# Kernel tuning notes

Measured on AMD Instinct MI355X. Metric: run time of the kernel, lower is better.

## Reference

```python
import jax, jax.numpy as jnp
import numpy as np

SEQ_LEN = 512
EMBED_DIM = 768
MAX_SPAN_LEN = 16
WIDTH_EMB_DIM = 50
NUM_SPAN_LABELS = 9
N_SPANS = 32768


def setup_inputs() -> dict:
    key = jax.random.key(0)
    ks = jax.random.split(key, 6)
    sequence_output = jax.random.normal(ks[0], (1, SEQ_LEN, EMBED_DIM), dtype=jnp.float32)
    # start in [0, SEQ_LEN - MAX_SPAN_LEN) so end = start + width stays a valid index
    start_indices = jax.random.randint(ks[1], (N_SPANS,), 0, SEQ_LEN - MAX_SPAN_LEN)
    span_widths = jax.random.randint(ks[2], (N_SPANS,), 1, MAX_SPAN_LEN + 1)  # width >= 1 (mean over non-empty slice)
    end_indices = start_indices + span_widths
    width_table = jax.random.normal(ks[3], (MAX_SPAN_LEN + 1, WIDTH_EMB_DIM), dtype=jnp.float32) * 0.02
    W = jax.random.normal(ks[4], (NUM_SPAN_LABELS, 3 * EMBED_DIM + WIDTH_EMB_DIM), dtype=jnp.float32) * 0.02
    b = jnp.zeros((NUM_SPAN_LABELS,), dtype=jnp.float32)
    return {
        "sequence_output": sequence_output,
        "start_indices": start_indices,
        "end_indices": end_indices,
        "span_widths": span_widths,
        "width_table": width_table,
        "W": W,
        "b": b,
    }


def reference(sequence_output, start_indices, end_indices, span_widths, width_table, W, b):
    # sequence_output: [1, S, D]; batch is asserted to be 1 in the original module.
    seq = sequence_output[0]                       # [S, D]
    h_start = seq[start_indices]                   # [N, D] gather of start tokens
    h_end = seq[end_indices]                       # [N, D] gather of end tokens
    # Ragged mean over seq[s:e] (exclusive end), vectorized via exclusive prefix sums:
    # mean = (cumsum[e] - cumsum[s]) / (e - s)
    cs = jnp.concatenate([jnp.zeros((1, seq.shape[-1]), seq.dtype), jnp.cumsum(seq, axis=0)], axis=0)  # [S+1, D]
    widths_f = span_widths[:, None].astype(seq.dtype)
    h_span_avg = (cs[end_indices] - cs[start_indices]) / widths_f   # [N, D]
    width_emb = width_table[span_widths]            # [N, 50]
    span_rep = jnp.concatenate([h_start, h_end, h_span_avg, width_emb], axis=-1)  # [N, 3D+50]
    logits = span_rep @ W.T + b                     # [N, num_labels]
    return logits
```

## Files before the change

kernel.cpp:

```cpp
#include <hip/hip_runtime.h>

#define SEQ_LEN 512
#define EMBED_DIM 768
#define WIDTH_EMB 50
#define NUM_LABELS 9
#define N_SPANS 32768
#define WROW (3 * EMBED_DIM + WIDTH_EMB)

#define P1_OFF 0
#define P2_OFF (SEQ_LEN * NUM_LABELS)
#define P3_OFF (2 * SEQ_LEN * NUM_LABELS)
#define C3_OFF (3 * SEQ_LEN * NUM_LABELS)
#define WP_OFF (C3_OFF + (SEQ_LEN + 1) * NUM_LABELS)

__global__ __launch_bounds__(576) void proj_kernel(
    const float* __restrict__ seq,
    const float* __restrict__ wtab,
    const float* __restrict__ W,
    const float* __restrict__ b,
    float* __restrict__ ws)
{
    const int blk = blockIdx.x;
    const int t   = threadIdx.x;

    if (blk < SEQ_LEN) {
        const int l    = t >> 6;
        const int lane = t & 63;

        const float2* srow = (const float2*)(seq + blk * EMBED_DIM);
        float2 s2[6];
#pragma unroll
        for (int k = 0; k < 6; ++k) s2[k] = srow[lane + 64 * k];

        const float2* wbase = (const float2*)(W + l * WROW);
        float p[3] = {0.f, 0.f, 0.f};
#pragma unroll
        for (int seg = 0; seg < 3; ++seg) {
#pragma unroll
            for (int k = 0; k < 6; ++k) {
                float2 wv = wbase[seg * 384 + lane + 64 * k];
                p[seg] += s2[k].x * wv.x + s2[k].y * wv.y;
            }
        }
#pragma unroll
        for (int seg = 0; seg < 3; ++seg) {
#pragma unroll
            for (int off = 32; off > 0; off >>= 1)
                p[seg] += __shfl_xor(p[seg], off, 64);
        }
        if (lane == 0) {
            ws[P1_OFF + blk * NUM_LABELS + l] = p[0];
            ws[P2_OFF + blk * NUM_LABELS + l] = p[1];
            ws[P3_OFF + blk * NUM_LABELS + l] = p[2];
        }
    } else {
        for (int idx = t; idx < 17 * NUM_LABELS; idx += 576) {
            int w = idx / NUM_LABELS;
            int l = idx - w * NUM_LABELS;
            const float* wrow = W + l * WROW + 3 * EMBED_DIM;
            const float* trow = wtab + w * WIDTH_EMB;
            float pp = b[l];
#pragma unroll
            for (int j = 0; j < WIDTH_EMB; ++j) pp += trow[j] * wrow[j];
            ws[WP_OFF + idx] = pp;
        }
    }
}

__global__ __launch_bounds__(576) void scan_kernel(float* __restrict__ ws)
{
    const int l    = threadIdx.x >> 6;
    const int lane = threadIdx.x & 63;

    float v[8];
#pragma unroll
    for (int j = 0; j < 8; ++j)
        v[j] = ws[P3_OFF + (lane * 8 + j) * NUM_LABELS + l];
#pragma unroll
    for (int j = 1; j < 8; ++j) v[j] += v[j - 1];

    const float lsum = v[7];
    float sc = lsum;
#pragma unroll
    for (int off = 1; off < 64; off <<= 1) {
        float u = __shfl_up(sc, off, 64);
        if (lane >= off) sc += u;
    }
    const float excl = sc - lsum;

#pragma unroll
    for (int j = 0; j < 8; ++j)
        ws[C3_OFF + (lane * 8 + j + 1) * NUM_LABELS + l] = excl + v[j];
    if (lane == 0) ws[C3_OFF + l] = 0.f;
}

#define SPB 64
__global__ __launch_bounds__(576) void span_kernel(
    const int* __restrict__ start_idx,
    const int* __restrict__ end_idx,
    const int* __restrict__ widths,
    const float* __restrict__ ws,
    float* __restrict__ out)
{
    const int t  = threadIdx.x;
    const int sp = t / NUM_LABELS;
    const int l  = t - sp * NUM_LABELS;
    const int n  = blockIdx.x * SPB + sp;

    const int s = start_idx[n];
    const int e = end_idx[n];
    const int w = widths[n];

    const float c = (ws[C3_OFF + e * NUM_LABELS + l]
                   - ws[C3_OFF + s * NUM_LABELS + l]) / (float)w;

    out[blockIdx.x * (SPB * NUM_LABELS) + t] =
          ws[P1_OFF + s * NUM_LABELS + l]
        + ws[P2_OFF + e * NUM_LABELS + l]
        + ws[WP_OFF + w * NUM_LABELS + l]
        + c;
}

extern "C" void kernel_launch(void* const* d_in, const int* in_sizes, int n_in,
                              void* d_out, int out_size, void* d_ws, size_t ws_size,
                              hipStream_t stream) {
    const float* seq  = (const float*)d_in[0];
    const int*   s    = (const int*)d_in[1];
    const int*   e    = (const int*)d_in[2];
    const int*   w    = (const int*)d_in[3];
    const float* wtab = (const float*)d_in[4];
    const float* W    = (const float*)d_in[5];
    const float* b    = (const float*)d_in[6];
    float* out = (float*)d_out;
    float* ws  = (float*)d_ws;

    proj_kernel<<<SEQ_LEN + 1, 576, 0, stream>>>(seq, wtab, W, b, ws);
    scan_kernel<<<1, 576, 0, stream>>>(ws);
    span_kernel<<<N_SPANS / SPB, 576, 0, stream>>>(s, e, w, ws, out);
}
```

Baseline: 78.03 us.

## Fuse prefix-scan into span kernel with LDS-staged projection tables

Removes the separate single-block scan kernel. Every span block now copies the per-token projection tables into shared memory, redundantly recomputes the prefix sum of the averaged-segment projection, and serves its gathers from LDS instead of global memory. This saves one kernel launch and the serial scan dependency. In exchange, each block repeats a ~55KB table load and scan, and the large shared-memory footprint limits occupancy.

```diff
diff --git a/kernel.cpp b/kernel.cpp
--- a/kernel.cpp
+++ b/kernel.cpp
@@ -10,10 +10,12 @@
 #define P1_OFF 0
 #define P2_OFF (SEQ_LEN * NUM_LABELS)
 #define P3_OFF (2 * SEQ_LEN * NUM_LABELS)
-#define C3_OFF (3 * SEQ_LEN * NUM_LABELS)
-#define WP_OFF (C3_OFF + (SEQ_LEN + 1) * NUM_LABELS)
+#define WP_OFF (3 * SEQ_LEN * NUM_LABELS)
 
-__global__ __launch_bounds__(576) void proj_kernel(
+#define SPB 64
+#define NTHREADS 576
+
+__global__ __launch_bounds__(NTHREADS) void proj_kernel(
     const float* __restrict__ seq,
     const float* __restrict__ wtab,
     const float* __restrict__ W,
@@ -54,7 +56,7 @@
             ws[P3_OFF + blk * NUM_LABELS + l] = p[2];
         }
     } else {
-        for (int idx = t; idx < 17 * NUM_LABELS; idx += 576) {
+        for (int idx = t; idx < 17 * NUM_LABELS; idx += NTHREADS) {
             int w = idx / NUM_LABELS;
             int l = idx - w * NUM_LABELS;
             const float* wrow = W + l * WROW + 3 * EMBED_DIM;
@@ -67,58 +69,66 @@
     }
 }
 
-__global__ __launch_bounds__(576) void scan_kernel(float* __restrict__ ws)
-{
-    const int l    = threadIdx.x >> 6;
-    const int lane = threadIdx.x & 63;
-
-    float v[8];
-#pragma unroll
-    for (int j = 0; j < 8; ++j)
-        v[j] = ws[P3_OFF + (lane * 8 + j) * NUM_LABELS + l];
-#pragma unroll
-    for (int j = 1; j < 8; ++j) v[j] += v[j - 1];
-
-    const float lsum = v[7];
-    float sc = lsum;
-#pragma unroll
-    for (int off = 1; off < 64; off <<= 1) {
-        float u = __shfl_up(sc, off, 64);
-        if (lane >= off) sc += u;
-    }
-    const float excl = sc - lsum;
-
-#pragma unroll
-    for (int j = 0; j < 8; ++j)
-        ws[C3_OFF + (lane * 8 + j + 1) * NUM_LABELS + l] = excl + v[j];
-    if (lane == 0) ws[C3_OFF + l] = 0.f;
-}
-
-#define SPB 64
-__global__ __launch_bounds__(576) void span_kernel(
+__global__ __launch_bounds__(NTHREADS) void span_kernel(
     const int* __restrict__ start_idx,
     const int* __restrict__ end_idx,
     const int* __restrict__ widths,
     const float* __restrict__ ws,
     float* __restrict__ out)
 {
-    const int t  = threadIdx.x;
-    const int sp = t / NUM_LABELS;
-    const int l  = t - sp * NUM_LABELS;
-    const int n  = blockIdx.x * SPB + sp;
+    __shared__ float sC3[(SEQ_LEN + 1) * NUM_LABELS];
+    __shared__ float sP1[SEQ_LEN * NUM_LABELS];
+    __shared__ float sP2[SEQ_LEN * NUM_LABELS];
+    __shared__ float sWP[17 * NUM_LABELS];
 
-    const int s = start_idx[n];
-    const int e = end_idx[n];
-    const int w = widths[n];
+    const int blk  = blockIdx.x;
+    const int t    = threadIdx.x;
+    const int l    = t >> 6;
+    const int lane = t & 63;
 
-    const float c = (ws[C3_OFF + e * NUM_LABELS + l]
-                   - ws[C3_OFF + s * NUM_LABELS + l]) / (float)w;
+    for (int i = t; i < SEQ_LEN * NUM_LABELS; i += NTHREADS) {
+        sP1[i] = ws[P1_OFF + i];
+        sP2[i] = ws[P2_OFF + i];
+        sC3[NUM_LABELS + i] = ws[P3_OFF + i];
+    }
+    if (t < 17 * NUM_LABELS) sWP[t] = ws[WP_OFF + t];
+    __syncthreads();
 
-    out[blockIdx.x * (SPB * NUM_LABELS) + t] =
-          ws[P1_OFF + s * NUM_LABELS + l]
-        + ws[P2_OFF + e * NUM_LABELS + l]
-        + ws[WP_OFF + w * NUM_LABELS + l]
-        + c;
+    {
+        float v[8];
+#pragma unroll
+        for (int j = 0; j < 8; ++j)
+            v[j] = sC3[NUM_LABELS + (lane * 8 + j) * NUM_LABELS + l];
+#pragma unroll
+        for (int j = 1; j < 8; ++j) v[j] += v[j - 1];
+        const float lsum = v[7];
+        float sc = lsum;
+#pragma unroll
+        for (int off = 1; off < 64; off <<= 1) {
+            float u = __shfl_up(sc, off, 64);
+            if (lane >= off) sc += u;
+        }
+        const float excl = sc - lsum;
+#pragma unroll
+        for (int j = 0; j < 8; ++j)
+            sC3[(lane * 8 + j + 1) * NUM_LABELS + l] = excl + v[j];
+        if (lane == 0) sC3[l] = 0.f;
+    }
+    __syncthreads();
+
+    {
+        const int sp = t / NUM_LABELS;
+        const int ll = t - sp * NUM_LABELS;
+        const int n  = blk * SPB + sp;
+        const int s  = start_idx[n];
+        const int e  = end_idx[n];
+        const int w  = widths[n];
+        out[blk * (SPB * NUM_LABELS) + t] =
+              sP1[s * NUM_LABELS + ll]
+            + sP2[e * NUM_LABELS + ll]
+            + sWP[w * NUM_LABELS + ll]
+            + (sC3[e * NUM_LABELS + ll] - sC3[s * NUM_LABELS + ll]) / (float)w;
+    }
 }
 
 extern "C" void kernel_launch(void* const* d_in, const int* in_sizes, int n_in,
@@ -134,7 +144,6 @@
     float* out = (float*)d_out;
     float* ws  = (float*)d_ws;
 
-    proj_kernel<<<SEQ_LEN + 1, 576, 0, stream>>>(seq, wtab, W, b, ws);
-    scan_kernel<<<1, 576, 0, stream>>>(ws);
-    span_kernel<<<N_SPANS / SPB, 576, 0, stream>>>(s, e, w, ws, out);
+    proj_kernel<<<SEQ_LEN + 1, NTHREADS, 0, stream>>>(seq, wtab, W, b, ws);
+    span_kernel<<<N_SPANS / SPB, NTHREADS, 0, stream>>>(s, e, w, ws, out);
 }
```

Result: no change. 77.08 us (-1.2%).
